# Kernel optimization log

Hardware: AMD Instinct MI355X
Metric: run time of the kernel (lower is better)

The kernel has to match this reference:

```python
import jax, jax.numpy as jnp
import numpy as np

N = 500_000
H_DIM = 256
G_DIM = 256
NUM_GRAPHS = 8192


def setup_inputs() -> dict:
    key = jax.random.key(0)
    k_h, k_b, k_w = jax.random.split(key, 3)
    h = jax.random.normal(k_h, (N, H_DIM), dtype=jnp.float32)
    batch = jnp.sort(jax.random.randint(k_b, (N,), 0, NUM_GRAPHS, dtype=jnp.int64))
    # Linear(h_dim*4, g_dim): weight [g_dim, 4*h_dim] in torch; we store as [4*h_dim, g_dim]
    fan_in = 4 * H_DIM
    bound = 1.0 / np.sqrt(fan_in)
    W = jax.random.uniform(k_w, (4 * H_DIM, G_DIM), minval=-bound, maxval=bound, dtype=jnp.float32)
    b = jnp.zeros((G_DIM,), dtype=jnp.float32)
    return {"h": h, "batch": batch, "W": W, "b": b, "num_graphs": NUM_GRAPHS}


def reference(h, batch, W, b, num_graphs):
    G = num_graphs
    ones = jnp.ones((h.shape[0],), dtype=h.dtype)
    cnt = jax.ops.segment_sum(ones, batch, num_segments=G)            # [G]
    s = jax.ops.segment_sum(h, batch, num_segments=G)                 # [G, D]
    ssq = jax.ops.segment_sum(h * h, batch, num_segments=G)           # [G, D]
    safe_cnt = jnp.maximum(cnt, 1.0)[:, None]
    h_mean = s / safe_cnt                                             # scatter mean (0 for empty)
    nonempty = (cnt > 0)[:, None]
    h_min = jnp.where(nonempty, jax.ops.segment_min(h, batch, num_segments=G), 0.0)
    h_max = jnp.where(nonempty, jax.ops.segment_max(h, batch, num_segments=G), 0.0)
    # unbiased std as in torch_scatter.scatter_std: var = (sum_sq - mean*sum) / (count - 1)
    var = (ssq - h_mean * s) / jnp.maximum(cnt - 1.0, 1.0)[:, None]
    h_std = jnp.sqrt(jnp.maximum(var, 0.0))
    hc = jnp.concatenate([h_mean, h_min, h_max, h_std], axis=1)       # [G, 4D]
    return hc @ W + b                                                 # [G, g_dim]
```

## Files before the change

### kernel.cpp

```cpp
#include <hip/hip_runtime.h>
#include <hip/hip_bf16.h>


#define DIM 256
#define NG 8192
#define KD 1024
#define NOUT 256

typedef __attribute__((ext_vector_type(8))) short bf16x8;
typedef __attribute__((ext_vector_type(4))) float f32x4;

__device__ __forceinline__ unsigned short f2bf(float x) {
    unsigned int u = __float_as_uint(x);
    u += 0x7fffu + ((u >> 16) & 1u);
    return (unsigned short)(u >> 16);
}

__global__ __launch_bounds__(256) void prep_kernel(const float* __restrict__ W,
                                                   const float* __restrict__ h,
                                                   const int* __restrict__ batch,
                                                   int N,
                                                   unsigned short* __restrict__ WT,
                                                   unsigned short* __restrict__ hc) {
    __shared__ float tile[64][68];

    if (blockIdx.x < 64) {
        const int t = threadIdx.x;
        const int tk0 = ((int)blockIdx.x & 15) * 64;
        const int tn0 = ((int)blockIdx.x >> 4) * 64;
        const int lk = t >> 2;
        const int ln = (t & 3) * 16;
#pragma unroll
        for (int j = 0; j < 16; j += 4) {
            float4 v = *(const float4*)&W[(size_t)(tk0 + lk) * NOUT + tn0 + ln + j];
            *(float4*)&tile[lk][ln + j] = v;
        }
        __syncthreads();
        const int on = t >> 2;
        const int ok = (t & 3) * 16;
        unsigned short tmp[16];
#pragma unroll
        for (int j = 0; j < 16; ++j) tmp[j] = f2bf(tile[ok + j][on]);
        const int n = tn0 + on;
        const int ct = n >> 4;
        const int c = n & 15;
        const int o0 = (tk0 + ok) >> 3;
        bf16x8 lo, hi;
#pragma unroll
        for (int j = 0; j < 8; ++j) { lo[j] = (short)tmp[j]; hi[j] = (short)tmp[8 + j]; }
        *(bf16x8*)&WT[(size_t)(((ct * 128 + o0) * 16 + c)) * 8]     = lo;
        *(bf16x8*)&WT[(size_t)(((ct * 128 + o0 + 1) * 16 + c)) * 8] = hi;
        return;
    }

    const int wave = threadIdx.x >> 6;
    const int lane = threadIdx.x & 63;
    const int g = (((int)blockIdx.x - 64) << 2) + wave;

    const bool is64 = (batch[N - 1] == 0);
    int target = g + (lane & 1);
    int lo = 0, hi = N;
    while (lo < hi) {
        int mid = (lo + hi) >> 1;
        int v = is64 ? batch[2 * mid] : batch[mid];
        if (v < target) lo = mid + 1; else hi = mid;
    }
    const int start = __shfl(lo, 0);
    const int end = __shfl(lo, 1);

    float s0[4] = {0.f, 0.f, 0.f, 0.f}, s1[4] = {0.f, 0.f, 0.f, 0.f};
    float q0[4] = {0.f, 0.f, 0.f, 0.f}, q1[4] = {0.f, 0.f, 0.f, 0.f};
    float mn[4] = {INFINITY, INFINITY, INFINITY, INFINITY};
    float mx[4] = {-INFINITY, -INFINITY, -INFINITY, -INFINITY};

    const f32x4* __restrict__ hv = (const f32x4*)h;
    int r = start;
    for (; r + 4 <= end; r += 4) {
        f32x4 A = __builtin_nontemporal_load(hv + (size_t)r * 64 + lane);
        f32x4 B = __builtin_nontemporal_load(hv + (size_t)(r + 1) * 64 + lane);
        f32x4 C = __builtin_nontemporal_load(hv + (size_t)(r + 2) * 64 + lane);
        f32x4 D = __builtin_nontemporal_load(hv + (size_t)(r + 3) * 64 + lane);
#pragma unroll
        for (int i = 0; i < 4; ++i) {
            s0[i] += A[i]; q0[i] = fmaf(A[i], A[i], q0[i]);
            mn[i] = fminf(mn[i], A[i]); mx[i] = fmaxf(mx[i], A[i]);
            s1[i] += B[i]; q1[i] = fmaf(B[i], B[i], q1[i]);
            mn[i] = fminf(mn[i], B[i]); mx[i] = fmaxf(mx[i], B[i]);
            s0[i] += C[i]; q0[i] = fmaf(C[i], C[i], q0[i]);
            mn[i] = fminf(mn[i], C[i]); mx[i] = fmaxf(mx[i], C[i]);
            s1[i] += D[i]; q1[i] = fmaf(D[i], D[i], q1[i]);
            mn[i] = fminf(mn[i], D[i]); mx[i] = fmaxf(mx[i], D[i]);
        }
    }
    for (; r < end; ++r) {
        f32x4 A = __builtin_nontemporal_load(hv + (size_t)r * 64 + lane);
#pragma unroll
        for (int i = 0; i < 4; ++i) {
            s0[i] += A[i]; q0[i] = fmaf(A[i], A[i], q0[i]);
            mn[i] = fminf(mn[i], A[i]); mx[i] = fmaxf(mx[i], A[i]);
        }
    }

    const int cnt = end - start;
    const float cf = (float)cnt;
    const float inv = cnt > 0 ? 1.f / cf : 0.f;
    const float invm1 = 1.f / fmaxf(cf - 1.f, 1.f);
    float mean[4], sd[4];
#pragma unroll
    for (int i = 0; i < 4; ++i) {
        float s = s0[i] + s1[i];
        float q = q0[i] + q1[i];
        mean[i] = s * inv;
        float var = (q - mean[i] * s) * invm1;
        sd[i] = sqrtf(fmaxf(var, 0.f));
        if (cnt == 0) { mn[i] = 0.f; mx[i] = 0.f; }
    }

    const int gt = g >> 4;
    const int gr = g & 15;
    ushort4* hc4 = (ushort4*)hc;
    const size_t base = ((size_t)gt * 128) ;
    const int oo = (lane >> 1);
    const int half = lane & 1;
#define STORE_STAT(st, v)                                                         \
    hc4[(((base + (st) * 32 + oo) * 16 + gr) << 1) + half] =                      \
        make_ushort4(f2bf(v[0]), f2bf(v[1]), f2bf(v[2]), f2bf(v[3]))
    STORE_STAT(0, mean);
    STORE_STAT(1, mn);
    STORE_STAT(2, mx);
    STORE_STAT(3, sd);
#undef STORE_STAT
}

__global__ __launch_bounds__(256) void gemm_kernel(const unsigned short* __restrict__ A,
                                                   const unsigned short* __restrict__ BT,
                                                   const float* __restrict__ bias,
                                                   float* __restrict__ out) {
    const int wave = threadIdx.x >> 6;
    const int lane = threadIdx.x & 63;
    const int r  = lane & 15;
    const int gq = lane >> 4;

    f32x4 acc[4] = {{0.f,0.f,0.f,0.f},{0.f,0.f,0.f,0.f},{0.f,0.f,0.f,0.f},{0.f,0.f,0.f,0.f}};

    const unsigned short* Ab = A + ((((size_t)blockIdx.x * 128 + gq) * 16 + r) << 3);
    const unsigned short* Bb[4];
#pragma unroll
    for (int fc = 0; fc < 4; ++fc)
        Bb[fc] = BT + ((((size_t)(wave * 4 + fc) * 128 + gq) * 16 + r) << 3);

#pragma unroll 2
    for (int t = 0; t < 32; ++t) {
        bf16x8 af = *(const bf16x8*)(Ab + t * 512);
#pragma unroll
        for (int fc = 0; fc < 4; ++fc) {
            bf16x8 bfr = *(const bf16x8*)(Bb[fc] + t * 512);
            acc[fc] = __builtin_amdgcn_mfma_f32_16x16x32_bf16(af, bfr, acc[fc], 0, 0, 0);
        }
    }

    const size_t row0 = (size_t)blockIdx.x * 16;
#pragma unroll
    for (int fc = 0; fc < 4; ++fc) {
        int col = wave * 64 + fc * 16 + r;
        float bv = bias[col];
#pragma unroll
        for (int e = 0; e < 4; ++e) {
            size_t row = row0 + gq * 4 + e;
            out[row * NOUT + col] = acc[fc][e] + bv;
        }
    }
}

extern "C" void kernel_launch(void* const* d_in, const int* in_sizes, int n_in,
                              void* d_out, int out_size, void* d_ws, size_t ws_size,
                              hipStream_t stream) {
    const float* h     = (const float*)d_in[0];
    const int*   batch = (const int*)d_in[1];
    const float* W     = (const float*)d_in[2];
    const float* b     = (const float*)d_in[3];
    float* out = (float*)d_out;

    const int N = in_sizes[0] / DIM;

    char* ws = (char*)d_ws;
    unsigned short* WT = (unsigned short*)ws;
    unsigned short* hc = (unsigned short*)(ws + 524288);

    prep_kernel<<<64 + NG / 4, 256, 0, stream>>>(W, h, batch, N, WT, hc);
    gemm_kernel<<<NG / 16, 256, 0, stream>>>(hc, WT, b, out);
}
```

Before: 118.7 us.

## Fuse segment statistics into GEMM kernel via swizzled LDS tile

Moves the segment-offset binary search into a small prep kernel that writes an offsets array, then fuses the per-graph statistics pass with the GEMM. Each 512-thread block reduces 32 graphs into a swizzled LDS tile of bf16 features and runs MFMA directly from LDS, removing the global hc round trip. The trade-off is only 256 blocks for streaming about 512 MB of h, so there is less parallelism for the memory-bound reduction, which may hurt bandwidth utilisation.

After: 100.8 us. -15.1%, faster.

```diff
diff --git a/kernel.cpp b/kernel.cpp
--- a/kernel.cpp
+++ b/kernel.cpp
@@ -16,142 +16,157 @@
     return (unsigned short)(u >> 16);
 }
 
+__device__ __forceinline__ unsigned int pack2(float a, float b) {
+    return (unsigned int)f2bf(a) | ((unsigned int)f2bf(b) << 16);
+}
+
 __global__ __launch_bounds__(256) void prep_kernel(const float* __restrict__ W,
-                                                   const float* __restrict__ h,
                                                    const int* __restrict__ batch,
                                                    int N,
                                                    unsigned short* __restrict__ WT,
-                                                   unsigned short* __restrict__ hc) {
+                                                   int* __restrict__ offs) {
     __shared__ float tile[64][68];
 
-    if (blockIdx.x < 64) {
-        const int t = threadIdx.x;
-        const int tk0 = ((int)blockIdx.x & 15) * 64;
-        const int tn0 = ((int)blockIdx.x >> 4) * 64;
-        const int lk = t >> 2;
-        const int ln = (t & 3) * 16;
-#pragma unroll
-        for (int j = 0; j < 16; j += 4) {
-            float4 v = *(const float4*)&W[(size_t)(tk0 + lk) * NOUT + tn0 + ln + j];
-            *(float4*)&tile[lk][ln + j] = v;
-        }
-        __syncthreads();
-        const int on = t >> 2;
-        const int ok = (t & 3) * 16;
-        unsigned short tmp[16];
-#pragma unroll
-        for (int j = 0; j < 16; ++j) tmp[j] = f2bf(tile[ok + j][on]);
-        const int n = tn0 + on;
-        const int ct = n >> 4;
-        const int c = n & 15;
-        const int o0 = (tk0 + ok) >> 3;
-        bf16x8 lo, hi;
-#pragma unroll
-        for (int j = 0; j < 8; ++j) { lo[j] = (short)tmp[j]; hi[j] = (short)tmp[8 + j]; }
-        *(bf16x8*)&WT[(size_t)(((ct * 128 + o0) * 16 + c)) * 8]     = lo;
-        *(bf16x8*)&WT[(size_t)(((ct * 128 + o0 + 1) * 16 + c)) * 8] = hi;
+    if (blockIdx.x >= 64) {
+        int t = ((int)blockIdx.x - 64) * 256 + (int)threadIdx.x;
+        if (t > NG) return;
+        const bool is64 = (batch[N - 1] == 0);
+        int lo = 0, hi = N;
+        while (lo < hi) {
+            int mid = (lo + hi) >> 1;
+            int v = is64 ? batch[2 * mid] : batch[mid];
+            if (v < t) lo = mid + 1; else hi = mid;
+        }
+        offs[t] = lo;
         return;
     }
 
-    const int wave = threadIdx.x >> 6;
+    const int t = threadIdx.x;
+    const int tk0 = ((int)blockIdx.x & 15) * 64;
+    const int tn0 = ((int)blockIdx.x >> 4) * 64;
+    const int lk = t >> 2;
+    const int ln = (t & 3) * 16;
+#pragma unroll
+    for (int j = 0; j < 16; j += 4) {
+        float4 v = *(const float4*)&W[(size_t)(tk0 + lk) * NOUT + tn0 + ln + j];
+        *(float4*)&tile[lk][ln + j] = v;
+    }
+    __syncthreads();
+    const int on = t >> 2;
+    const int ok = (t & 3) * 16;
+    unsigned short tmp[16];
+#pragma unroll
+    for (int j = 0; j < 16; ++j) tmp[j] = f2bf(tile[ok + j][on]);
+    const int n = tn0 + on;
+    const int ct = n >> 4;
+    const int c = n & 15;
+    const int o0 = (tk0 + ok) >> 3;
+    bf16x8 lo8, hi8;
+#pragma unroll
+    for (int j = 0; j < 8; ++j) { lo8[j] = (short)tmp[j]; hi8[j] = (short)tmp[8 + j]; }
+    *(bf16x8*)&WT[(size_t)(((ct * 128 + o0) * 16 + c)) * 8]     = lo8;
+    *(bf16x8*)&WT[(size_t)(((ct * 128 + o0 + 1) * 16 + c)) * 8] = hi8;
+}
+
+__global__ __launch_bounds__(512) void fused_kernel(const float* __restrict__ h,
+                                                    const int* __restrict__ offs,
+                                                    const unsigned short* __restrict__ BT,
+                                                    const float* __restrict__ bias,
+                                                    float* __restrict__ out) {
+    __shared__ unsigned short As[32 * 1024];
+    const int w = threadIdx.x >> 6;
     const int lane = threadIdx.x & 63;
-    const int g = (((int)blockIdx.x - 64) << 2) + wave;
-
-    const bool is64 = (batch[N - 1] == 0);
-    int target = g + (lane & 1);
-    int lo = 0, hi = N;
-    while (lo < hi) {
-        int mid = (lo + hi) >> 1;
-        int v = is64 ? batch[2 * mid] : batch[mid];
-        if (v < target) lo = mid + 1; else hi = mid;
-    }
-    const int start = __shfl(lo, 0);
-    const int end = __shfl(lo, 1);
-
-    float s0[4] = {0.f, 0.f, 0.f, 0.f}, s1[4] = {0.f, 0.f, 0.f, 0.f};
-    float q0[4] = {0.f, 0.f, 0.f, 0.f}, q1[4] = {0.f, 0.f, 0.f, 0.f};
-    float mn[4] = {INFINITY, INFINITY, INFINITY, INFINITY};
-    float mx[4] = {-INFINITY, -INFINITY, -INFINITY, -INFINITY};
-
+    const int tile = blockIdx.x;
+    const int g0 = tile * 32 + w * 4;
+
+    const int ob = offs[g0 + (lane < 5 ? lane : 4)];
     const f32x4* __restrict__ hv = (const f32x4*)h;
-    int r = start;
-    for (; r + 4 <= end; r += 4) {
-        f32x4 A = __builtin_nontemporal_load(hv + (size_t)r * 64 + lane);
-        f32x4 B = __builtin_nontemporal_load(hv + (size_t)(r + 1) * 64 + lane);
-        f32x4 C = __builtin_nontemporal_load(hv + (size_t)(r + 2) * 64 + lane);
-        f32x4 D = __builtin_nontemporal_load(hv + (size_t)(r + 3) * 64 + lane);
-#pragma unroll
-        for (int i = 0; i < 4; ++i) {
-            s0[i] += A[i]; q0[i] = fmaf(A[i], A[i], q0[i]);
-            mn[i] = fminf(mn[i], A[i]); mx[i] = fmaxf(mx[i], A[i]);
-            s1[i] += B[i]; q1[i] = fmaf(B[i], B[i], q1[i]);
-            mn[i] = fminf(mn[i], B[i]); mx[i] = fmaxf(mx[i], B[i]);
-            s0[i] += C[i]; q0[i] = fmaf(C[i], C[i], q0[i]);
-            mn[i] = fminf(mn[i], C[i]); mx[i] = fmaxf(mx[i], C[i]);
-            s1[i] += D[i]; q1[i] = fmaf(D[i], D[i], q1[i]);
-            mn[i] = fminf(mn[i], D[i]); mx[i] = fmaxf(mx[i], D[i]);
-        }
-    }
-    for (; r < end; ++r) {
-        f32x4 A = __builtin_nontemporal_load(hv + (size_t)r * 64 + lane);
-#pragma unroll
-        for (int i = 0; i < 4; ++i) {
-            s0[i] += A[i]; q0[i] = fmaf(A[i], A[i], q0[i]);
-            mn[i] = fminf(mn[i], A[i]); mx[i] = fmaxf(mx[i], A[i]);
-        }
-    }
-
-    const int cnt = end - start;
-    const float cf = (float)cnt;
-    const float inv = cnt > 0 ? 1.f / cf : 0.f;
-    const float invm1 = 1.f / fmaxf(cf - 1.f, 1.f);
-    float mean[4], sd[4];
-#pragma unroll
+
     for (int i = 0; i < 4; ++i) {
-        float s = s0[i] + s1[i];
-        float q = q0[i] + q1[i];
-        mean[i] = s * inv;
-        float var = (q - mean[i] * s) * invm1;
-        sd[i] = sqrtf(fmaxf(var, 0.f));
-        if (cnt == 0) { mn[i] = 0.f; mx[i] = 0.f; }
-    }
-
-    const int gt = g >> 4;
-    const int gr = g & 15;
-    ushort4* hc4 = (ushort4*)hc;
-    const size_t base = ((size_t)gt * 128) ;
-    const int oo = (lane >> 1);
-    const int half = lane & 1;
-#define STORE_STAT(st, v)                                                         \
-    hc4[(((base + (st) * 32 + oo) * 16 + gr) << 1) + half] =                      \
-        make_ushort4(f2bf(v[0]), f2bf(v[1]), f2bf(v[2]), f2bf(v[3]))
-    STORE_STAT(0, mean);
-    STORE_STAT(1, mn);
-    STORE_STAT(2, mx);
-    STORE_STAT(3, sd);
-#undef STORE_STAT
-}
-
-__global__ __launch_bounds__(256) void gemm_kernel(const unsigned short* __restrict__ A,
-                                                   const unsigned short* __restrict__ BT,
-                                                   const float* __restrict__ bias,
-                                                   float* __restrict__ out) {
-    const int wave = threadIdx.x >> 6;
-    const int lane = threadIdx.x & 63;
-    const int r  = lane & 15;
+        const int start = __shfl(ob, i);
+        const int end = __shfl(ob, i + 1);
+
+        float s0[4] = {0.f,0.f,0.f,0.f}, s1[4] = {0.f,0.f,0.f,0.f};
+        float q0[4] = {0.f,0.f,0.f,0.f}, q1[4] = {0.f,0.f,0.f,0.f};
+        float mn[4] = {INFINITY, INFINITY, INFINITY, INFINITY};
+        float mx[4] = {-INFINITY, -INFINITY, -INFINITY, -INFINITY};
+
+        int r = start;
+        for (; r + 8 <= end; r += 8) {
+            f32x4 v[8];
+#pragma unroll
+            for (int j = 0; j < 8; ++j)
+                v[j] = __builtin_nontemporal_load(hv + (size_t)(r + j) * 64 + lane);
+#pragma unroll
+            for (int j = 0; j < 8; ++j) {
+                if (j & 1) {
+#pragma unroll
+                    for (int i2 = 0; i2 < 4; ++i2) {
+                        s1[i2] += v[j][i2]; q1[i2] = fmaf(v[j][i2], v[j][i2], q1[i2]);
+                        mn[i2] = fminf(mn[i2], v[j][i2]); mx[i2] = fmaxf(mx[i2], v[j][i2]);
+                    }
+                } else {
+#pragma unroll
+                    for (int i2 = 0; i2 < 4; ++i2) {
+                        s0[i2] += v[j][i2]; q0[i2] = fmaf(v[j][i2], v[j][i2], q0[i2]);
+                        mn[i2] = fminf(mn[i2], v[j][i2]); mx[i2] = fmaxf(mx[i2], v[j][i2]);
+                    }
+                }
+            }
+        }
+        for (; r < end; ++r) {
+            f32x4 a = __builtin_nontemporal_load(hv + (size_t)r * 64 + lane);
+#pragma unroll
+            for (int i2 = 0; i2 < 4; ++i2) {
+                s0[i2] += a[i2]; q0[i2] = fmaf(a[i2], a[i2], q0[i2]);
+                mn[i2] = fminf(mn[i2], a[i2]); mx[i2] = fmaxf(mx[i2], a[i2]);
+            }
+        }
+
+        const int cnt = end - start;
+        const float cf = (float)cnt;
+        const float inv = cnt > 0 ? 1.f / cf : 0.f;
+        const float invm1 = 1.f / fmaxf(cf - 1.f, 1.f);
+        float mean[4], sd[4];
+#pragma unroll
+        for (int i2 = 0; i2 < 4; ++i2) {
+            float s = s0[i2] + s1[i2];
+            float q = q0[i2] + q1[i2];
+            mean[i2] = s * inv;
+            float var = (q - mean[i2] * s) * invm1;
+            sd[i2] = sqrtf(fmaxf(var, 0.f));
+            if (cnt == 0) { mn[i2] = 0.f; mx[i2] = 0.f; }
+        }
+
+        const int lr = w * 4 + i;
+        const unsigned int rx = (unsigned int)((lr & 7) << 4);
+        char* base = (char*)As;
+        const unsigned int b0 = (unsigned int)(lr * 2048 + lane * 8);
+        *(uint2*)(base + ((b0 + 0)    ^ rx)) = make_uint2(pack2(mean[0], mean[1]), pack2(mean[2], mean[3]));
+        *(uint2*)(base + ((b0 + 512)  ^ rx)) = make_uint2(pack2(mn[0], mn[1]),     pack2(mn[2], mn[3]));
+        *(uint2*)(base + ((b0 + 1024) ^ rx)) = make_uint2(pack2(mx[0], mx[1]),     pack2(mx[2], mx[3]));
+        *(uint2*)(base + ((b0 + 1536) ^ rx)) = make_uint2(pack2(sd[0], sd[1]),     pack2(sd[2], sd[3]));
+    }
+
+    __syncthreads();
+
+    const int wr = w >> 2, wc = w & 3;
+    const int fr = lane & 15;
     const int gq = lane >> 4;
+    const int rowr = wr * 16 + fr;
+    const unsigned int arx = (unsigned int)((fr & 7) << 4);
+    const unsigned int abase = (unsigned int)(rowr * 2048 + gq * 16);
 
     f32x4 acc[4] = {{0.f,0.f,0.f,0.f},{0.f,0.f,0.f,0.f},{0.f,0.f,0.f,0.f},{0.f,0.f,0.f,0.f}};
 
-    const unsigned short* Ab = A + ((((size_t)blockIdx.x * 128 + gq) * 16 + r) << 3);
     const unsigned short* Bb[4];
 #pragma unroll
     for (int fc = 0; fc < 4; ++fc)
-        Bb[fc] = BT + ((((size_t)(wave * 4 + fc) * 128 + gq) * 16 + r) << 3);
+        Bb[fc] = BT + ((((size_t)(wc * 4 + fc) * 128 + gq) * 16 + fr) << 3);
 
 #pragma unroll 2
     for (int t = 0; t < 32; ++t) {
-        bf16x8 af = *(const bf16x8*)(Ab + t * 512);
+        bf16x8 af = *(const bf16x8*)((const char*)As + ((abase + t * 64) ^ arx));
 #pragma unroll
         for (int fc = 0; fc < 4; ++fc) {
             bf16x8 bfr = *(const bf16x8*)(Bb[fc] + t * 512);
@@ -159,14 +174,14 @@
         }
     }
 
-    const size_t row0 = (size_t)blockIdx.x * 16;
+    const size_t row0 = (size_t)tile * 32;
 #pragma unroll
     for (int fc = 0; fc < 4; ++fc) {
-        int col = wave * 64 + fc * 16 + r;
+        int col = wc * 64 + fc * 16 + fr;
         float bv = bias[col];
 #pragma unroll
         for (int e = 0; e < 4; ++e) {
-            size_t row = row0 + gq * 4 + e;
+            size_t row = row0 + wr * 16 + gq * 4 + e;
             out[row * NOUT + col] = acc[fc][e] + bv;
         }
     }
@@ -185,8 +200,8 @@
 
     char* ws = (char*)d_ws;
     unsigned short* WT = (unsigned short*)ws;
-    unsigned short* hc = (unsigned short*)(ws + 524288);
-
-    prep_kernel<<<64 + NG / 4, 256, 0, stream>>>(W, h, batch, N, WT, hc);
-    gemm_kernel<<<NG / 16, 256, 0, stream>>>(hc, WT, b, out);
-}
+    int* offs = (int*)(ws + 524288);
+
+    prep_kernel<<<97, 256, 0, stream>>>(W, batch, N, WT, offs);
+    fused_kernel<<<256, 512, 0, stream>>>(h, offs, WT, b, out);
+}
```
